# Optimization experiments

Hardware: AMD Instinct MI355X
Metric: run time of the kernel (lower is better)

## Reference

```python
import jax, jax.numpy as jnp
import numpy as np

N, E = 50000, 800000
C_IN, C_OUT, DIM, K = 64, 64, 3, 2
EPS = 1e-5


def setup_inputs() -> dict:
    key = jax.random.key(0)
    k1, k2, k3, k4, k5 = jax.random.split(key, 5)
    x = jax.random.normal(k1, (N, C_IN), dtype=jnp.float32)
    edge_index = jax.random.randint(k2, (2, E), 0, N, dtype=jnp.int32)
    edge_attr = jax.random.uniform(k3, (E, DIM), dtype=jnp.float32)  # pseudo coords in [0,1]
    W = jax.random.normal(k4, (K ** DIM, C_IN, C_OUT), dtype=jnp.float32) * 0.05
    root = jax.random.normal(k5, (C_IN, C_OUT), dtype=jnp.float32) * 0.05
    gamma = jnp.ones((C_OUT,), dtype=jnp.float32)
    beta = jnp.zeros((C_OUT,), dtype=jnp.float32)
    return {"x": x, "edge_attr": edge_attr, "W": W, "root": root,
            "gamma": gamma, "beta": beta, "edge_index": edge_index}


def _spline_basis(edge_attr):
    """Degree-1 open B-spline basis. Returns (weights [E,2^D], kernel idx [E,2^D])."""
    D = edge_attr.shape[1]
    v = edge_attr * (K - 1)                      # [E, D]
    k0 = jnp.floor(v)
    frac = v - k0                                # in [0,1)
    k0 = k0.astype(jnp.int32)
    bits = np.stack(np.unravel_index(np.arange(2 ** D), (2,) * D), axis=-1).astype(np.int32)  # [2^D, D]
    bits_f = jnp.asarray(bits, dtype=edge_attr.dtype)
    # per-dim weight: frac if bit else (1 - frac); product over dims
    w = jnp.where(bits_f[None] > 0, frac[:, None, :], 1.0 - frac[:, None, :])  # [E, 2^D, D]
    weights = jnp.prod(w, axis=-1)               # [E, 2^D]
    idx_d = jnp.clip(k0[:, None, :] + bits[None], 0, K - 1)  # [E, 2^D, D]
    radix = jnp.asarray(K ** np.arange(D), dtype=jnp.int32)
    idx = jnp.sum(idx_d * radix, axis=-1)        # [E, 2^D] in [0, K^D)
    return weights, idx


def reference(x, edge_attr, W, root, gamma, beta, edge_index):
    src, dst = edge_index[0], edge_index[1]
    Etot = edge_attr.shape[0]
    S = W.shape[0]  # K^D

    weights, idx = _spline_basis(edge_attr)      # [E, 2^D] each
    # dense per-edge basis over all K^D kernel slots
    B = jnp.zeros((Etot, S), dtype=x.dtype).at[jnp.arange(Etot)[:, None], idx].add(weights)

    xj = x[src]                                  # [E, C_in] gather
    z = (B[:, :, None] * xj[:, None, :]).reshape(Etot, S * x.shape[1])  # [E, S*C_in]
    msg = z @ W.reshape(S * x.shape[1], W.shape[2])                     # [E, C_out]

    agg = jax.ops.segment_sum(msg, dst, num_segments=x.shape[0])        # scatter-add
    cnt = jax.ops.segment_sum(jnp.ones((Etot,), dtype=x.dtype), dst, num_segments=x.shape[0])
    out = agg / jnp.maximum(cnt, 1.0)[:, None] + x @ root               # mean aggr + root weight

    # BatchNorm over nodes (training-mode batch stats)
    mean = jnp.mean(out, axis=0)
    var = jnp.var(out, axis=0)
    y = (out - mean) * jax.lax.rsqrt(var + EPS) * gamma + beta
    return jax.nn.elu(y)
```

## Files before the change

kernel.cpp:

```cpp
#include <hip/hip_runtime.h>
#include <hip/hip_bf16.h>
#include <cstdint>
#include <cstddef>

#define NN 50000
#define NE 800000
#define EPS 1e-5f

typedef short bf16x8 __attribute__((ext_vector_type(8)));
typedef float f32x4  __attribute__((ext_vector_type(4)));
typedef float f32x2  __attribute__((ext_vector_type(2)));


#define NB_WT   144
#define NB_CNT  3125
#define NB_MFMA 782
#define NB_SCAN 25

static __device__ __forceinline__ ushort f2bf(float f) {
    __hip_bfloat16 h = __float2bfloat16(f);
    return *reinterpret_cast<ushort*>(&h);
}
static __device__ __forceinline__ float bf_lo(uint32_t u) {
    return __uint_as_float(u << 16);
}
static __device__ __forceinline__ float bf_hi(uint32_t u) {
    return __uint_as_float(u & 0xffff0000u);
}
static __device__ __forceinline__ uint32_t pack2(float a, float b) {
    return (uint32_t)f2bf(a) | ((uint32_t)f2bf(b) << 16);
}

__global__ __launch_bounds__(256) void prep_count_k(const float* __restrict__ W,
                                                    const float* __restrict__ root,
                                                    ushort* __restrict__ WTg,
                                                    const int* __restrict__ ei,
                                                    int* __restrict__ deg,
                                                    int* __restrict__ rank,
                                                    float* __restrict__ bnps,
                                                    float* __restrict__ bnpq) {
    const int b = blockIdx.x;
    if (b < NB_WT) {
        const int idx = b * 256 + threadIdx.x;
        const int s  = idx >> 12;
        const int co = (idx >> 6) & 63;
        const int ci = idx & 63;
        const float v = (s < 8) ? W[s * 4096 + ci * 64 + co] : root[ci * 64 + co];
        WTg[idx] = f2bf(v);
        if (idx < 4096) { bnps[idx] = 0.f; bnpq[idx] = 0.f; }
    } else {
        const int e = (b - NB_WT) * 256 + threadIdx.x;
        if (e < NE) rank[e] = atomicAdd(&deg[ei[NE + e]], 1);
    }
}

__global__ __launch_bounds__(256) void mfma_scan_k(
        const float* __restrict__ x, const ushort* __restrict__ WTg,
        uint8_t* __restrict__ H8, ushort* __restrict__ Hrootb,
        const int* __restrict__ deg, int* __restrict__ offs,
        int* __restrict__ part) {
    __shared__ __align__(16) ushort XA[64 * 64];
    __shared__ __align__(16) ushort WT[5 * 64 * 64];
    __shared__ int sh[256];
    const int t = threadIdx.x;
    const int b = blockIdx.x;

    if (b >= NB_MFMA) {
        const int sb = b - NB_MFMA;
        const int base = sb * 2048 + t * 8;
        int v[8]; int sum = 0;
        #pragma unroll
        for (int k = 0; k < 8; ++k) {
            int i = base + k;
            int d = (i < NN) ? deg[i] : 0;
            v[k] = sum; sum += d;
        }
        sh[t] = sum; __syncthreads();
        for (int off = 1; off < 256; off <<= 1) {
            int val = sh[t];
            int add = (t >= off) ? sh[t - off] : 0;
            __syncthreads();
            sh[t] = val + add;
            __syncthreads();
        }
        int excl = (t > 0) ? sh[t - 1] : 0;
        #pragma unroll
        for (int k = 0; k < 8; ++k) {
            int i = base + k;
            if (i < NN) offs[i] = excl + v[k];
        }
        if (t == 255) part[sb] = sh[255];
        return;
    }

    const int n0 = b * 64;

    #pragma unroll
    for (int rep = 0; rep < 2; ++rep) {
        const int vt   = rep * 256 + t;
        const int row  = vt >> 3;
        const int col8 = vt & 7;
        const int n = n0 + row;
        uint4 u;
        if (n < NN) {
            const float4 v0 = *(const float4*)&x[(size_t)n * 64 + col8 * 8];
            const float4 v1 = *(const float4*)&x[(size_t)n * 64 + col8 * 8 + 4];
            u.x = pack2(v0.x, v0.y); u.y = pack2(v0.z, v0.w);
            u.z = pack2(v1.x, v1.y); u.w = pack2(v1.z, v1.w);
        } else {
            u = make_uint4(0, 0, 0, 0);
        }
        const int idx = (row * 64 + col8 * 8) ^ ((row & 7) << 3);
        *(uint4*)&XA[idx] = u;
    }

    const int w    = t >> 6;
    const int lane = t & 63;
    const int mrow = lane & 15;
    const int kgrp = lane >> 4;
    const int swz  = (mrow & 7) << 3;
    const int arow = w * 16 + mrow;
    const int n    = n0 + arow;
    bf16x8 a0, a1;

    for (int pass = 0; pass < 2; ++pass) {
        const int sbeg   = pass ? 5 : 0;
        const int scount = pass ? 4 : 5;
        const int nchunk = scount * 512;
        for (int c = t; c < nchunk; c += 256) {
            const int row  = c >> 3;
            const int col8 = c & 7;
            const uint4 u = *(const uint4*)&WTg[(size_t)(sbeg * 64 + row) * 64 + col8 * 8];
            const int idx = (row * 64 + col8 * 8) ^ ((row & 7) << 3);
            *(uint4*)&WT[idx] = u;
        }
        __syncthreads();
        if (pass == 0) {
            a0 = *(const bf16x8*)&XA[((arow * 64) + 0 * 32 + kgrp * 8) ^ swz];
            a1 = *(const bf16x8*)&XA[((arow * 64) + 1 * 32 + kgrp * 8) ^ swz];
        }
        for (int sl = 0; sl < scount; ++sl) {
            const int s = sbeg + sl;
            const ushort* wt = &WT[sl * 4096];
            f32x4 acc[4];
            #pragma unroll
            for (int ct = 0; ct < 4; ++ct) {
                acc[ct] = (f32x4){0.f, 0.f, 0.f, 0.f};
                const int brow = ct * 16 + mrow;
                const bf16x8 b0 = *(const bf16x8*)&wt[((brow * 64) + 0 * 32 + kgrp * 8) ^ swz];
                const bf16x8 b1 = *(const bf16x8*)&wt[((brow * 64) + 1 * 32 + kgrp * 8) ^ swz];
                acc[ct] = __builtin_amdgcn_mfma_f32_16x16x32_bf16(b0, a0, acc[ct], 0, 0, 0);
                acc[ct] = __builtin_amdgcn_mfma_f32_16x16x32_bf16(b1, a1, acc[ct], 0, 0, 0);
            }
            if (n < NN) {
                if (s < 8) {
                    #pragma unroll
                    for (int ct = 0; ct < 4; ++ct) {
                        int p = __builtin_amdgcn_cvt_pk_fp8_f32(acc[ct][0], acc[ct][1], 0, false);
                        p     = __builtin_amdgcn_cvt_pk_fp8_f32(acc[ct][2], acc[ct][3], p, true);
                        *(uint32_t*)&H8[(size_t)n * 512 + s * 64 + ct * 16 + kgrp * 4] = (uint32_t)p;
                    }
                } else {
                    #pragma unroll
                    for (int ct = 0; ct < 4; ++ct) {
                        ushort4 h4;
                        h4.x = f2bf(acc[ct][0]); h4.y = f2bf(acc[ct][1]);
                        h4.z = f2bf(acc[ct][2]); h4.w = f2bf(acc[ct][3]);
                        *(ushort4*)&Hrootb[(size_t)n * 64 + ct * 16 + kgrp * 4] = h4;
                    }
                }
            }
        }
        __syncthreads();
    }
}

__global__ __launch_bounds__(256) void scatter_k(const int* __restrict__ ei,
                                                 const float* __restrict__ attr,
                                                 const int* __restrict__ offs,
                                                 const int* __restrict__ part,
                                                 const int* __restrict__ rank,
                                                 int2* __restrict__ recs) {
    __shared__ int pp[25];
    const int t = threadIdx.x;
    if (t < 25) pp[t] = part[t];
    __syncthreads();
    if (t == 0) {
        int s = 0;
        #pragma unroll
        for (int i = 0; i < 25; ++i) { int v = pp[i]; pp[i] = s; s += v; }
    }
    __syncthreads();
    int e = blockIdx.x * 256 + t;
    if (e >= NE) return;
    const int src = ei[e];
    const int dst = ei[NE + e];
    const float f0 = attr[(size_t)e * 3 + 0];
    const float f1 = attr[(size_t)e * 3 + 1];
    const float f2 = attr[(size_t)e * 3 + 2];
    const uint32_t q = (uint32_t)rintf(f0 * 1023.f)
                     | ((uint32_t)rintf(f1 * 1023.f) << 10)
                     | ((uint32_t)rintf(f2 * 1023.f) << 20);
    const int p = offs[dst] + pp[dst >> 11] + rank[e];
    recs[p] = make_int2(src, (int)q);
}

__global__ __launch_bounds__(256) void aggregate_k(const int* __restrict__ offs,
                                                   const int* __restrict__ part,
                                                   const int* __restrict__ deg,
                                                   const int2* __restrict__ recs,
                                                   const uint8_t* __restrict__ H8,
                                                   const ushort* __restrict__ Hrootb,
                                                   float* __restrict__ outb,
                                                   float* __restrict__ bnps,
                                                   float* __restrict__ bnpq) {
    __shared__ int pp[25];
    __shared__ float red_s[4][64], red_q[4][64];
    const int t = threadIdx.x, lane = t & 63, w = t >> 6;
    if (t < 25) pp[t] = part[t];
    __syncthreads();
    if (t == 0) {
        int s = 0;
        #pragma unroll
        for (int i = 0; i < 25; ++i) { int v = pp[i]; pp[i] = s; s += v; }
    }
    __syncthreads();

    const int n = blockIdx.x * 4 + w;
    const int sidx = lane >> 3;
    const int cog  = lane & 7;
    const float sg0 = (sidx & 1) ? 1.f : -1.f, cc0 = (sidx & 1) ? 0.f : 1.f;
    const float sg1 = (sidx & 2) ? 1.f : -1.f, cc1 = (sidx & 2) ? 0.f : 1.f;
    const float sg2 = (sidx & 4) ? 1.f : -1.f, cc2 = (sidx & 4) ? 0.f : 1.f;
    const int cnt = deg[n];
    const int beg = offs[n] + pp[n >> 11];
    const int2* rp = recs + beg;
    const size_t loff = (size_t)(lane << 3);

    f32x2 acc2[4] = {(f32x2){0.f, 0.f}, (f32x2){0.f, 0.f},
                     (f32x2){0.f, 0.f}, (f32x2){0.f, 0.f}};

#define DECODE_W(qv, wv)                                                     \
    {                                                                        \
        const uint32_t q_ = (uint32_t)(qv);                                  \
        const float f0_ = (float)(q_ & 1023u) * (1.f / 1023.f);              \
        const float f1_ = (float)((q_ >> 10) & 1023u) * (1.f / 1023.f);      \
        const float f2_ = (float)((q_ >> 20) & 1023u) * (1.f / 1023.f);      \
        wv = (cc0 + sg0 * f0_) * ((cc1 + sg1 * f1_) * (cc2 + sg2 * f2_));    \
    }
#define ACCUM(wv, h)                                                         \
    {                                                                        \
        const f32x2 w2_ = {wv, wv};                                          \
        acc2[0] += w2_ * (f32x2)__builtin_amdgcn_cvt_pk_f32_fp8((int)(h).x, false); \
        acc2[1] += w2_ * (f32x2)__builtin_amdgcn_cvt_pk_f32_fp8((int)(h).x, true);  \
        acc2[2] += w2_ * (f32x2)__builtin_amdgcn_cvt_pk_f32_fp8((int)(h).y, false); \
        acc2[3] += w2_ * (f32x2)__builtin_amdgcn_cvt_pk_f32_fp8((int)(h).y, true);  \
    }

    int j = 0;
    for (; j + 3 < cnt; j += 4) {
        const int2 r0 = rp[j];
        const int2 r1 = rp[j + 1];
        const int2 r2 = rp[j + 2];
        const int2 r3 = rp[j + 3];
        const uint2 h0 = *(const uint2*)(H8 + (size_t)r0.x * 512 + loff);
        const uint2 h1 = *(const uint2*)(H8 + (size_t)r1.x * 512 + loff);
        const uint2 h2 = *(const uint2*)(H8 + (size_t)r2.x * 512 + loff);
        const uint2 h3 = *(const uint2*)(H8 + (size_t)r3.x * 512 + loff);
        float w0, w1, w2, w3;
        DECODE_W(r0.y, w0); DECODE_W(r1.y, w1);
        DECODE_W(r2.y, w2); DECODE_W(r3.y, w3);
        ACCUM(w0, h0); ACCUM(w1, h1); ACCUM(w2, h2); ACCUM(w3, h3);
    }
    for (; j < cnt; ++j) {
        const int2 r0 = rp[j];
        const uint2 h0 = *(const uint2*)(H8 + (size_t)r0.x * 512 + loff);
        float w0;
        DECODE_W(r0.y, w0);
        ACCUM(w0, h0);
    }
#undef DECODE_W
#undef ACCUM

    float accf[8] = {acc2[0].x, acc2[0].y, acc2[1].x, acc2[1].y,
                     acc2[2].x, acc2[2].y, acc2[3].x, acc2[3].y};
    #pragma unroll
    for (int k = 0; k < 8; ++k) {
        float v = accf[k];
        v += __shfl_xor(v, 8, 64);
        v += __shfl_xor(v, 16, 64);
        v += __shfl_xor(v, 32, 64);
        accf[k] = v;
    }
    if (sidx == 0) {
        const float inv = 1.f / fmaxf((float)cnt, 1.f);
        const size_t base = (size_t)n * 64 + cog * 8;
        const uint4 hr = *(const uint4*)&Hrootb[base];
        const float rr[8] = {bf_lo(hr.x), bf_hi(hr.x), bf_lo(hr.y), bf_hi(hr.y),
                             bf_lo(hr.z), bf_hi(hr.z), bf_lo(hr.w), bf_hi(hr.w)};
        float vv[8];
        #pragma unroll
        for (int k = 0; k < 8; ++k) vv[k] = accf[k] * inv + rr[k];
        *(float4*)&outb[base]     = make_float4(vv[0], vv[1], vv[2], vv[3]);
        *(float4*)&outb[base + 4] = make_float4(vv[4], vv[5], vv[6], vv[7]);
        #pragma unroll
        for (int k = 0; k < 8; ++k) {
            red_s[w][k * 8 + cog] = vv[k];
            red_q[w][k * 8 + cog] = vv[k] * vv[k];
        }
    }
    __syncthreads();
    if (t < 64) {
        const float s = red_s[0][t] + red_s[1][t] + red_s[2][t] + red_s[3][t];
        const float q = red_q[0][t] + red_q[1][t] + red_q[2][t] + red_q[3][t];
        const int co = (t & 7) * 8 + (t >> 3);
        const int slot = (blockIdx.x & 63) * 64 + co;
        atomicAdd(&bnps[slot], s);
        atomicAdd(&bnpq[slot], q);
    }
}

__global__ __launch_bounds__(256) void finalize_kernel(float* __restrict__ outb,
                                                       const float* __restrict__ bnps,
                                                       const float* __restrict__ bnpq,
                                                       const float* __restrict__ gamma,
                                                       const float* __restrict__ beta) {
    __shared__ float sc_sh[64], sh_sh[64];
    const int t = threadIdx.x;
    if (t < 64) {
        float s = 0.f, q = 0.f;
        for (int k = 0; k < 64; ++k) { s += bnps[k * 64 + t]; q += bnpq[k * 64 + t]; }
        const float mean = s * (1.f / NN);
        const float var  = q * (1.f / NN) - mean * mean;
        const float sc = rsqrtf(var + EPS) * gamma[t];
        sc_sh[t] = sc;
        sh_sh[t] = beta[t] - mean * sc;
    }
    __syncthreads();
    const int total4 = NN * 16;
    for (int idx = blockIdx.x * 256 + t; idx < total4; idx += gridDim.x * 256) {
        float4 v = ((const float4*)outb)[idx];
        const int co0 = (idx & 15) * 4;
        float o[4] = {v.x, v.y, v.z, v.w};
        #pragma unroll
        for (int j = 0; j < 4; ++j) {
            const float y = o[j] * sc_sh[co0 + j] + sh_sh[co0 + j];
            o[j] = (y > 0.f) ? y : expm1f(y);
        }
        ((float4*)outb)[idx] = make_float4(o[0], o[1], o[2], o[3]);
    }
}

extern "C" void kernel_launch(void* const* d_in, const int* in_sizes, int n_in,
                              void* d_out, int out_size, void* d_ws, size_t ws_size,
                              hipStream_t stream) {
    const float* x     = (const float*)d_in[0];
    const float* attr  = (const float*)d_in[1];
    const float* W     = (const float*)d_in[2];
    const float* root  = (const float*)d_in[3];
    const float* gamma = (const float*)d_in[4];
    const float* beta  = (const float*)d_in[5];
    const int*   ei    = (const int*)d_in[6];
    float* outb = (float*)d_out;

    char* ws = (char*)d_ws;
    uint8_t* H8     = (uint8_t*)(ws);
    ushort*  Hrootb = (ushort*)(ws + 25600000);
    int2*    recs   = (int2*)(ws + 32000000);
    int*     rank   = (int*)(ws + 38400000);
    int*     offs   = (int*)(ws + 41600000);
    int*     deg    = (int*)(ws + 41800000);
    int*     part   = (int*)(ws + 42000000);
    float*   bnps   = (float*)(ws + 42000128);
    float*   bnpq   = (float*)(ws + 42016512);
    ushort*  WTg    = (ushort*)(ws + 42032896);

    hipMemsetAsync(ws + 41800000, 0, 200128, stream);

    prep_count_k<<<NB_WT + NB_CNT, 256, 0, stream>>>(W, root, WTg, ei, deg, rank, bnps, bnpq);
    mfma_scan_k<<<NB_MFMA + NB_SCAN, 256, 0, stream>>>(x, WTg, H8, Hrootb, deg, offs, part);
    scatter_k<<<NB_CNT, 256, 0, stream>>>(ei, attr, offs, part, rank, recs);
    aggregate_k<<<NN / 4, 256, 0, stream>>>(offs, part, deg, recs, H8, Hrootb, outb, bnps, bnpq);
    finalize_kernel<<<256, 256, 0, stream>>>(outb, bnps, bnpq, gamma, beta);
}
```

Baseline: 167.8 us.

## Split scan into own kernel, fuse edge scatter with MFMA transform, nontemporal accesses

Moves the degree prefix scan into a small standalone kernel and merges the edge scatter into the MFMA feature-transform launch, so scatter blocks run alongside the GEMM blocks instead of in a separate launch afterwards. Record writes and reads, root-term loads and output stores now use nontemporal builtins to reduce cache pollution. The cost is an extra tiny launch, and the fused kernel's scatter blocks reserve the large LDS footprint of the MFMA path, which may limit how many scatter blocks are resident at once.

```diff
diff --git a/kernel.cpp b/kernel.cpp
--- a/kernel.cpp
+++ b/kernel.cpp
@@ -10,6 +10,8 @@
 typedef short bf16x8 __attribute__((ext_vector_type(8)));
 typedef float f32x4  __attribute__((ext_vector_type(4)));
 typedef float f32x2  __attribute__((ext_vector_type(2)));
+typedef unsigned int u32x4 __attribute__((ext_vector_type(4)));
+typedef float fv4 __attribute__((ext_vector_type(4)));
 
 
 #define NB_WT   144
@@ -54,42 +56,71 @@
     }
 }
 
-__global__ __launch_bounds__(256) void mfma_scan_k(
+__global__ __launch_bounds__(256) void scan_k(const int* __restrict__ deg,
+                                              int* __restrict__ offs,
+                                              int* __restrict__ part) {
+    __shared__ int sh[256];
+    const int b = blockIdx.x, t = threadIdx.x;
+    const int base = b * 2048 + t * 8;
+    int v[8]; int sum = 0;
+    #pragma unroll
+    for (int k = 0; k < 8; ++k) {
+        int i = base + k;
+        int d = (i < NN) ? deg[i] : 0;
+        v[k] = sum; sum += d;
+    }
+    sh[t] = sum; __syncthreads();
+    for (int off = 1; off < 256; off <<= 1) {
+        int val = sh[t];
+        int add = (t >= off) ? sh[t - off] : 0;
+        __syncthreads();
+        sh[t] = val + add;
+        __syncthreads();
+    }
+    int excl = (t > 0) ? sh[t - 1] : 0;
+    #pragma unroll
+    for (int k = 0; k < 8; ++k) {
+        int i = base + k;
+        if (i < NN) offs[i] = excl + v[k];
+    }
+    if (t == 255) part[b] = sh[255];
+}
+
+__global__ __launch_bounds__(256) void mfma_scatter_k(
         const float* __restrict__ x, const ushort* __restrict__ WTg,
         uint8_t* __restrict__ H8, ushort* __restrict__ Hrootb,
-        const int* __restrict__ deg, int* __restrict__ offs,
-        int* __restrict__ part) {
+        const int* __restrict__ ei, const float* __restrict__ attr,
+        const int* __restrict__ offs, const int* __restrict__ part,
+        const int* __restrict__ rank, int2* __restrict__ recs) {
     __shared__ __align__(16) ushort XA[64 * 64];
     __shared__ __align__(16) ushort WT[5 * 64 * 64];
-    __shared__ int sh[256];
+    __shared__ int pp[25];
     const int t = threadIdx.x;
     const int b = blockIdx.x;
 
     if (b >= NB_MFMA) {
-        const int sb = b - NB_MFMA;
-        const int base = sb * 2048 + t * 8;
-        int v[8]; int sum = 0;
-        #pragma unroll
-        for (int k = 0; k < 8; ++k) {
-            int i = base + k;
-            int d = (i < NN) ? deg[i] : 0;
-            v[k] = sum; sum += d;
-        }
-        sh[t] = sum; __syncthreads();
-        for (int off = 1; off < 256; off <<= 1) {
-            int val = sh[t];
-            int add = (t >= off) ? sh[t - off] : 0;
-            __syncthreads();
-            sh[t] = val + add;
-            __syncthreads();
-        }
-        int excl = (t > 0) ? sh[t - 1] : 0;
-        #pragma unroll
-        for (int k = 0; k < 8; ++k) {
-            int i = base + k;
-            if (i < NN) offs[i] = excl + v[k];
-        }
-        if (t == 255) part[sb] = sh[255];
+        if (t < 25) pp[t] = part[t];
+        __syncthreads();
+        if (t == 0) {
+            int s = 0;
+            #pragma unroll
+            for (int i = 0; i < 25; ++i) { int v = pp[i]; pp[i] = s; s += v; }
+        }
+        __syncthreads();
+        const int e = (b - NB_MFMA) * 256 + t;
+        if (e >= NE) return;
+        const int src = ei[e];
+        const int dst = ei[NE + e];
+        const float f0 = attr[(size_t)e * 3 + 0];
+        const float f1 = attr[(size_t)e * 3 + 1];
+        const float f2 = attr[(size_t)e * 3 + 2];
+        const uint32_t q = (uint32_t)rintf(f0 * 1023.f)
+                         | ((uint32_t)rintf(f1 * 1023.f) << 10)
+                         | ((uint32_t)rintf(f2 * 1023.f) << 20);
+        const int p = offs[dst] + pp[dst >> 11] + rank[e];
+        const unsigned long long rec =
+            (unsigned long long)(uint32_t)src | ((unsigned long long)q << 32);
+        __builtin_nontemporal_store(rec, (unsigned long long*)&recs[p]);
         return;
     }
 
@@ -175,36 +206,6 @@
     }
 }
 
-__global__ __launch_bounds__(256) void scatter_k(const int* __restrict__ ei,
-                                                 const float* __restrict__ attr,
-                                                 const int* __restrict__ offs,
-                                                 const int* __restrict__ part,
-                                                 const int* __restrict__ rank,
-                                                 int2* __restrict__ recs) {
-    __shared__ int pp[25];
-    const int t = threadIdx.x;
-    if (t < 25) pp[t] = part[t];
-    __syncthreads();
-    if (t == 0) {
-        int s = 0;
-        #pragma unroll
-        for (int i = 0; i < 25; ++i) { int v = pp[i]; pp[i] = s; s += v; }
-    }
-    __syncthreads();
-    int e = blockIdx.x * 256 + t;
-    if (e >= NE) return;
-    const int src = ei[e];
-    const int dst = ei[NE + e];
-    const float f0 = attr[(size_t)e * 3 + 0];
-    const float f1 = attr[(size_t)e * 3 + 1];
-    const float f2 = attr[(size_t)e * 3 + 2];
-    const uint32_t q = (uint32_t)rintf(f0 * 1023.f)
-                     | ((uint32_t)rintf(f1 * 1023.f) << 10)
-                     | ((uint32_t)rintf(f2 * 1023.f) << 20);
-    const int p = offs[dst] + pp[dst >> 11] + rank[e];
-    recs[p] = make_int2(src, (int)q);
-}
-
 __global__ __launch_bounds__(256) void aggregate_k(const int* __restrict__ offs,
                                                    const int* __restrict__ part,
                                                    const int* __restrict__ deg,
@@ -240,6 +241,13 @@
     f32x2 acc2[4] = {(f32x2){0.f, 0.f}, (f32x2){0.f, 0.f},
                      (f32x2){0.f, 0.f}, (f32x2){0.f, 0.f}};
 
+#define LOAD_REC(jj, sv, qv)                                                 \
+    {                                                                        \
+        const unsigned long long rr_ =                                       \
+            __builtin_nontemporal_load((const unsigned long long*)(rp + (jj))); \
+        sv = (int)(uint32_t)rr_;                                             \
+        qv = (uint32_t)(rr_ >> 32);                                          \
+    }
 #define DECODE_W(qv, wv)                                                     \
     {                                                                        \
         const uint32_t q_ = (uint32_t)(qv);                                  \
@@ -259,26 +267,27 @@
 
     int j = 0;
     for (; j + 3 < cnt; j += 4) {
-        const int2 r0 = rp[j];
-        const int2 r1 = rp[j + 1];
-        const int2 r2 = rp[j + 2];
-        const int2 r3 = rp[j + 3];
-        const uint2 h0 = *(const uint2*)(H8 + (size_t)r0.x * 512 + loff);
-        const uint2 h1 = *(const uint2*)(H8 + (size_t)r1.x * 512 + loff);
-        const uint2 h2 = *(const uint2*)(H8 + (size_t)r2.x * 512 + loff);
-        const uint2 h3 = *(const uint2*)(H8 + (size_t)r3.x * 512 + loff);
+        int s0, s1, s2, s3; uint32_t q0, q1, q2, q3;
+        LOAD_REC(j, s0, q0); LOAD_REC(j + 1, s1, q1);
+        LOAD_REC(j + 2, s2, q2); LOAD_REC(j + 3, s3, q3);
+        const uint2 h0 = *(const uint2*)(H8 + (size_t)s0 * 512 + loff);
+        const uint2 h1 = *(const uint2*)(H8 + (size_t)s1 * 512 + loff);
+        const uint2 h2 = *(const uint2*)(H8 + (size_t)s2 * 512 + loff);
+        const uint2 h3 = *(const uint2*)(H8 + (size_t)s3 * 512 + loff);
         float w0, w1, w2, w3;
-        DECODE_W(r0.y, w0); DECODE_W(r1.y, w1);
-        DECODE_W(r2.y, w2); DECODE_W(r3.y, w3);
+        DECODE_W(q0, w0); DECODE_W(q1, w1);
+        DECODE_W(q2, w2); DECODE_W(q3, w3);
         ACCUM(w0, h0); ACCUM(w1, h1); ACCUM(w2, h2); ACCUM(w3, h3);
     }
     for (; j < cnt; ++j) {
-        const int2 r0 = rp[j];
-        const uint2 h0 = *(const uint2*)(H8 + (size_t)r0.x * 512 + loff);
+        int s0; uint32_t q0;
+        LOAD_REC(j, s0, q0);
+        const uint2 h0 = *(const uint2*)(H8 + (size_t)s0 * 512 + loff);
         float w0;
-        DECODE_W(r0.y, w0);
+        DECODE_W(q0, w0);
         ACCUM(w0, h0);
     }
+#undef LOAD_REC
 #undef DECODE_W
 #undef ACCUM
 
@@ -295,14 +304,16 @@
     if (sidx == 0) {
         const float inv = 1.f / fmaxf((float)cnt, 1.f);
         const size_t base = (size_t)n * 64 + cog * 8;
-        const uint4 hr = *(const uint4*)&Hrootb[base];
+        const u32x4 hr = __builtin_nontemporal_load((const u32x4*)&Hrootb[base]);
         const float rr[8] = {bf_lo(hr.x), bf_hi(hr.x), bf_lo(hr.y), bf_hi(hr.y),
                              bf_lo(hr.z), bf_hi(hr.z), bf_lo(hr.w), bf_hi(hr.w)};
         float vv[8];
         #pragma unroll
         for (int k = 0; k < 8; ++k) vv[k] = accf[k] * inv + rr[k];
-        *(float4*)&outb[base]     = make_float4(vv[0], vv[1], vv[2], vv[3]);
-        *(float4*)&outb[base + 4] = make_float4(vv[4], vv[5], vv[6], vv[7]);
+        const fv4 o0 = {vv[0], vv[1], vv[2], vv[3]};
+        const fv4 o1 = {vv[4], vv[5], vv[6], vv[7]};
+        __builtin_nontemporal_store(o0, (fv4*)&outb[base]);
+        __builtin_nontemporal_store(o1, (fv4*)&outb[base + 4]);
         #pragma unroll
         for (int k = 0; k < 8; ++k) {
             red_s[w][k * 8 + cog] = vv[k];
@@ -378,8 +389,9 @@
     hipMemsetAsync(ws + 41800000, 0, 200128, stream);
 
     prep_count_k<<<NB_WT + NB_CNT, 256, 0, stream>>>(W, root, WTg, ei, deg, rank, bnps, bnpq);
-    mfma_scan_k<<<NB_MFMA + NB_SCAN, 256, 0, stream>>>(x, WTg, H8, Hrootb, deg, offs, part);
-    scatter_k<<<NB_CNT, 256, 0, stream>>>(ei, attr, offs, part, rank, recs);
+    scan_k<<<NB_SCAN, 256, 0, stream>>>(deg, offs, part);
+    mfma_scatter_k<<<NB_MFMA + NB_CNT, 256, 0, stream>>>(x, WTg, H8, Hrootb,
+                                                         ei, attr, offs, part, rank, recs);
     aggregate_k<<<NN / 4, 256, 0, stream>>>(offs, part, deg, recs, H8, Hrootb, outb, bnps, bnpq);
     finalize_kernel<<<256, 256, 0, stream>>>(outb, bnps, bnpq, gamma, beta);
 }
```

Result: slower. 182.0 us (+8.5%).
